# Kernel optimization log

Hardware: AMD Instinct MI355X
Metric: run time of the kernel (lower is better)

The kernel has to match this reference:

```python
import jax, jax.numpy as jnp
import numpy as np

HIDDEN = 2048
NUM_HEADS = 16
HEAD_DIM = HIDDEN // NUM_HEADS


def setup_inputs() -> dict:
    key = jax.random.key(0)
    ks = jax.random.split(key, 5)
    B, S, H = 2, 2048, HIDDEN
    # xavier_uniform bounds
    qkv_bound = float(np.sqrt(6.0 / (H + 3 * H)))
    out_bound = float(np.sqrt(6.0 / (H + H)))
    return {
        "x": jax.random.normal(ks[0], (B, S, H), dtype=jnp.float32),
        "W_qkv": jax.random.uniform(ks[1], (3 * H, H), minval=-qkv_bound, maxval=qkv_bound, dtype=jnp.float32),
        "b_qkv": jnp.zeros((3 * H,), dtype=jnp.float32),
        "W_out": jax.random.uniform(ks[2], (H, H), minval=-out_bound, maxval=out_bound, dtype=jnp.float32),
        "b_out": jnp.zeros((H,), dtype=jnp.float32),
    }


def reference(x, W_qkv, b_qkv, W_out, b_out):
    B, S, H = x.shape
    # fused QKV projection (torch Linear: x @ W.T + b)
    qkv = x @ W_qkv.T + b_qkv                      # (B, S, 3H)
    q, k, v = jnp.split(qkv, 3, axis=-1)
    # (B, S, H) -> (B, N, S, D)
    def to_heads(t):
        return t.reshape(B, S, NUM_HEADS, HEAD_DIM).transpose(0, 2, 1, 3)
    q, k, v = to_heads(q), to_heads(k), to_heads(v)
    scale = HEAD_DIM ** -0.5
    scores = jnp.einsum("bnqd,bnkd->bnqk", q, k) * scale  # (B, N, S, S)
    causal = jnp.triu(jnp.ones((S, S), dtype=bool), k=1)
    scores = jnp.where(causal, -jnp.inf, scores)
    attn = jax.nn.softmax(scores, axis=-1)
    out = jnp.einsum("bnqk,bnkd->bnqd", attn, v)           # (B, N, S, D)
    out = out.transpose(0, 2, 1, 3).reshape(B, S, H)
    return out @ W_out.T + b_out
```

## Files before the change

kernel.cpp:

```cpp
#include <hip/hip_runtime.h>
#include <stdint.h>


using bf16x8 = __attribute__((ext_vector_type(8))) __bf16;
using f32x4  = __attribute__((ext_vector_type(4))) float;

#define S_LEN 2048
#define HID   2048
#define NHEAD 16
#define DHEAD 128
#define QSCALE_L2E (0.08838834764831845f * 1.4426950408889634f)

__device__ __forceinline__ unsigned short f2bf(float f) {
  union { float f; unsigned int u; } c; c.f = f;
  unsigned int u = c.u;
  return (unsigned short)((u + 0x7FFFu + ((u >> 16) & 1u)) >> 16);
}

__device__ __forceinline__ unsigned int pkbf(float a, float b) {
  union { __bf16 h[2]; unsigned int u; } x;
  x.h[0] = (__bf16)a; x.h[1] = (__bf16)b;
  return x.u;
}

__device__ __forceinline__ void gload_lds16(const void* g, void* l) {
  __builtin_amdgcn_global_load_lds(
      (const __attribute__((address_space(1))) unsigned int*)g,
      (__attribute__((address_space(3))) unsigned int*)l, 16, 0, 0);
}

__device__ __forceinline__ f32x4 mfma16(bf16x8 a, bf16x8 b, f32x4 c) {
  return __builtin_amdgcn_mfma_f32_16x16x32_bf16(a, b, c, 0, 0, 0);
}

__device__ __forceinline__ float hmax4(f32x4 v) {
  return fmaxf(fmaxf(v[0], v[1]), fmaxf(v[2], v[3]));
}

__global__ void cvt_bf16(const float* __restrict__ in, unsigned short* __restrict__ out, int n) {
  const int n4 = n >> 2;
  const int stride = gridDim.x * blockDim.x;
  for (int i = blockIdx.x * blockDim.x + threadIdx.x; i < n4; i += stride) {
    float4 v = reinterpret_cast<const float4*>(in)[i];
    ushort4 o;
    o.x = f2bf(v.x); o.y = f2bf(v.y); o.z = f2bf(v.z); o.w = f2bf(v.w);
    reinterpret_cast<ushort4*>(out)[i] = o;
  }
}

template<int EPI>
__global__ __launch_bounds__(256) void gemm_bt(
    const unsigned short* __restrict__ A, const unsigned short* __restrict__ Bw,
    const float* __restrict__ bias, int K, int N,
    unsigned short* __restrict__ q_out, unsigned short* __restrict__ k_out,
    unsigned short* __restrict__ vt_out, float* __restrict__ c_out)
{
  __shared__ char lsA[128 * 128];
  __shared__ char lsB[128 * 128];
  const int tid = threadIdx.x;
  const int l = tid & 63, w = tid >> 6;
  const int wr = w >> 1, wc = w & 1;
  const int bm = blockIdx.x * 128, bn = blockIdx.y * 128;
  const int row16 = l & 15, kg = l >> 4;

  f32x4 acc[4][4] = {};

  for (int k0 = 0; k0 < K; k0 += 64) {
    #pragma unroll
    for (int c = 0; c < 4; ++c) {
      const int o = c * 4096 + tid * 16;
      const int r = o >> 7;
      const int cb = (o & 127) ^ ((r & 7) << 4);
      gload_lds16((const char*)A + ((size_t)(bm + r) * K + k0) * 2 + cb,
                  lsA + c * 4096 + (w << 10));
      gload_lds16((const char*)Bw + ((size_t)(bn + r) * K + k0) * 2 + cb,
                  lsB + c * 4096 + (w << 10));
    }
    __syncthreads();

    #pragma unroll
    for (int h = 0; h < 2; ++h) {
      bf16x8 af[4], bfr[4];
      #pragma unroll
      for (int i = 0; i < 4; ++i) {
        const int ra = wr * 64 + i * 16 + row16;
        af[i]  = *(const bf16x8*)(lsA + ra * 128 + ((h * 64 + kg * 16) ^ ((ra & 7) << 4)));
        const int rb = wc * 64 + i * 16 + row16;
        bfr[i] = *(const bf16x8*)(lsB + rb * 128 + ((h * 64 + kg * 16) ^ ((rb & 7) << 4)));
      }
      #pragma unroll
      for (int i = 0; i < 4; ++i)
        #pragma unroll
        for (int j = 0; j < 4; ++j)
          acc[i][j] = mfma16(af[i], bfr[j], acc[i][j]);
    }
    __syncthreads();
  }

  const int r0 = kg * 4;
  #pragma unroll
  for (int i = 0; i < 4; ++i) {
    const int row = bm + wr * 64 + i * 16 + r0;
    #pragma unroll
    for (int j = 0; j < 4; ++j) {
      const int col = bn + wc * 64 + j * 16 + row16;
      const float bv = bias[col];
      if (EPI == 1) {
        #pragma unroll
        for (int r = 0; r < 4; ++r)
          c_out[(size_t)(row + r) * N + col] = acc[i][j][r] + bv;
      } else {
        const int sec = col >> 11;
        const int within = col & 2047;
        const int head = within >> 7, d = within & 127;
        #pragma unroll
        for (int r = 0; r < 4; ++r) {
          const int rr = row + r;
          const int b = rr >> 11, s = rr & 2047;
          const int bh = b * NHEAD + head;
          const float v = acc[i][j][r] + bv;
          if (sec == 0)
            q_out[((size_t)bh * S_LEN + s) * DHEAD + d] = f2bf(v * QSCALE_L2E);
          else if (sec == 1)
            k_out[((size_t)bh * S_LEN + s) * DHEAD + d] = f2bf(v);
          else
            vt_out[((size_t)bh * DHEAD + d) * S_LEN + s] = f2bf(v);
        }
      }
    }
  }
}

__global__ __launch_bounds__(256, 2) void attn_fwd(
    const unsigned short* __restrict__ Q, const unsigned short* __restrict__ Kk,
    const unsigned short* __restrict__ Vt, unsigned short* __restrict__ O)
{
  __shared__ char lsK[2][64 * 256];
  __shared__ char lsV[2][128 * 128];
  __shared__ char lsP[4][32 * 128];
  const int tid = threadIdx.x, l = tid & 63, w = tid >> 6;
  const int row16 = l & 15, kg = l >> 4;
  const int qb = (blockIdx.y < 16) ? (15 - (int)blockIdx.x) : (int)blockIdx.x;
  const int bh = blockIdx.y;
  const int bidx = bh >> 4, head = bh & 15;

  const char* Qh = (const char*)(Q  + (size_t)bh * S_LEN * DHEAD);
  const char* Kh = (const char*)(Kk + (size_t)bh * S_LEN * DHEAD);
  const char* Vh = (const char*)(Vt + (size_t)bh * DHEAD * S_LEN);

  const int q0w = qb * 128 + w * 32;

  bf16x8 qf[2][4];
  #pragma unroll
  for (int qs = 0; qs < 2; ++qs)
    #pragma unroll
    for (int t = 0; t < 4; ++t)
      qf[qs][t] = *(const bf16x8*)(Qh + ((size_t)(q0w + qs * 16 + row16) * DHEAD + t * 32 + kg * 8) * 2);

  float m[2]  = {-1e30f, -1e30f};
  float ls[2] = {0.f, 0.f};
  f32x4 oacc[2][8] = {};

  const int last = 2 * qb + 1;

#define STAGE(buf, kt_) do {                                                     \
    _Pragma("unroll")                                                            \
    for (int c = 0; c < 4; ++c) {                                                \
      const int o = c * 4096 + tid * 16;                                         \
      const int rk = o >> 8, cbk = (o & 255) ^ ((rk & 7) << 4);                  \
      gload_lds16(Kh + (size_t)((kt_) * 64 + rk) * 256 + cbk,                    \
                  lsK[buf] + c * 4096 + (w << 10));                              \
      const int dv = o >> 7, cbv = (o & 127) ^ ((dv & 7) << 4);                  \
      gload_lds16(Vh + (size_t)dv * 4096 + (size_t)(kt_) * 128 + cbv,            \
                  lsV[buf] + c * 4096 + (w << 10));                              \
    } } while (0)

  STAGE(0, 0);
  __syncthreads();

  int cur = 0;
  for (int kt = 0; ; ++kt) {
    if (kt < last) STAGE(cur ^ 1, kt + 1);

    if (kt * 64 <= q0w + 31) {
      const char* Kc = lsK[cur];
      const char* Vc = lsV[cur];
      char* Pl = lsP[w];

      f32x4 sc[4][2] = {};
      #pragma unroll
      for (int j = 0; j < 4; ++j) {
        const int krow = j * 16 + row16;
        const int sw = (krow & 7) << 4;
        bf16x8 kf[4];
        #pragma unroll
        for (int t = 0; t < 4; ++t)
          kf[t] = *(const bf16x8*)(Kc + krow * 256 + ((t * 64 + kg * 16) ^ sw));
        #pragma unroll
        for (int t = 0; t < 4; ++t) {
          sc[j][0] = mfma16(kf[t], qf[0][t], sc[j][0]);
          sc[j][1] = mfma16(kf[t], qf[1][t], sc[j][1]);
        }
      }

      if (kt >= 2 * qb) {
        #pragma unroll
        for (int j = 0; j < 4; ++j) {
          const int kvb = kt * 64 + j * 16 + kg * 4;
          #pragma unroll
          for (int qs = 0; qs < 2; ++qs) {
            const int qq = q0w + qs * 16 + row16;
            #pragma unroll
            for (int r = 0; r < 4; ++r)
              if (kvb + r > qq) sc[j][qs][r] = -1e30f;
          }
        }
      }

      float pm[2], al[2] = {1.f, 1.f};
      #pragma unroll
      for (int qs = 0; qs < 2; ++qs) {
        float mx = fmaxf(fmaxf(hmax4(sc[0][qs]), hmax4(sc[1][qs])),
                         fmaxf(hmax4(sc[2][qs]), hmax4(sc[3][qs])));
        mx = fmaxf(mx, __shfl_xor(mx, 16, 64));
        mx = fmaxf(mx, __shfl_xor(mx, 32, 64));
        pm[qs] = mx;
      }
      const bool need = (pm[0] > m[0] + 8.f) || (pm[1] > m[1] + 8.f);
      if (__any(need)) {
        const float n0 = fmaxf(m[0], pm[0]), n1 = fmaxf(m[1], pm[1]);
        al[0] = exp2f(m[0] - n0); al[1] = exp2f(m[1] - n1);
        m[0] = n0; m[1] = n1;
        float aq[2][4];
        #pragma unroll
        for (int qs2 = 0; qs2 < 2; ++qs2)
          #pragma unroll
          for (int r = 0; r < 4; ++r)
            aq[qs2][r] = __shfl(al[qs2], kg * 4 + r, 64);
        #pragma unroll
        for (int qs2 = 0; qs2 < 2; ++qs2)
          #pragma unroll
          for (int dt = 0; dt < 8; ++dt)
            #pragma unroll
            for (int r = 0; r < 4; ++r)
              oacc[qs2][dt][r] *= aq[qs2][r];
      }

      #pragma unroll
      for (int qs = 0; qs < 2; ++qs) {
        const int q = qs * 16 + row16;
        const int psw = (q & 7) << 4;
        float ps = 0.f;
        #pragma unroll
        for (int j = 0; j < 4; ++j) {
          const float p0 = exp2f(sc[j][qs][0] - m[qs]);
          const float p1 = exp2f(sc[j][qs][1] - m[qs]);
          const float p2 = exp2f(sc[j][qs][2] - m[qs]);
          const float p3 = exp2f(sc[j][qs][3] - m[qs]);
          ps += (p0 + p1) + (p2 + p3);
          uint2 pw; pw.x = pkbf(p0, p1); pw.y = pkbf(p2, p3);
          *(uint2*)(Pl + q * 128 + ((j * 32 + kg * 8) ^ psw)) = pw;
        }
        ps += __shfl_xor(ps, 16, 64);
        ps += __shfl_xor(ps, 32, 64);
        ls[qs] = ls[qs] * al[qs] + ps;
      }

      bf16x8 pa[2][2];
      #pragma unroll
      for (int qs2 = 0; qs2 < 2; ++qs2) {
        const int q = qs2 * 16 + row16;
        #pragma unroll
        for (int ks = 0; ks < 2; ++ks)
          pa[qs2][ks] = *(const bf16x8*)(Pl + q * 128 + ((ks * 64 + kg * 16) ^ ((q & 7) << 4)));
      }
      #pragma unroll
      for (int dt = 0; dt < 8; ++dt) {
        const int drow = dt * 16 + row16;
        const int vsw = (drow & 7) << 4;
        bf16x8 v0 = *(const bf16x8*)(Vc + drow * 128 + ((kg * 16) ^ vsw));
        bf16x8 v1 = *(const bf16x8*)(Vc + drow * 128 + ((64 + kg * 16) ^ vsw));
        oacc[0][dt] = mfma16(pa[0][0], v0, oacc[0][dt]);
        oacc[0][dt] = mfma16(pa[0][1], v1, oacc[0][dt]);
        oacc[1][dt] = mfma16(pa[1][0], v0, oacc[1][dt]);
        oacc[1][dt] = mfma16(pa[1][1], v1, oacc[1][dt]);
      }
    }

    __syncthreads();
    if (kt == last) break;
    cur ^= 1;
  }
#undef STAGE

  #pragma unroll
  for (int qs2 = 0; qs2 < 2; ++qs2) {
    #pragma unroll
    for (int r = 0; r < 4; ++r) {
      const float lr = __shfl(ls[qs2], kg * 4 + r, 64);
      const float inv = 1.0f / lr;
      const int q = q0w + qs2 * 16 + kg * 4 + r;
      const size_t orow = (size_t)(bidx * S_LEN + q) * HID + (size_t)head * DHEAD;
      #pragma unroll
      for (int dt = 0; dt < 8; ++dt)
        O[orow + dt * 16 + row16] = f2bf(oacc[qs2][dt][r] * inv);
    }
  }
}

extern "C" void kernel_launch(void* const* d_in, const int* in_sizes, int n_in,
                              void* d_out, int out_size, void* d_ws, size_t ws_size,
                              hipStream_t stream) {
  const float* x    = (const float*)d_in[0];
  const float* Wqkv = (const float*)d_in[1];
  const float* bqkv = (const float*)d_in[2];
  const float* Wout = (const float*)d_in[3];
  const float* bout = (const float*)d_in[4];
  float* out = (float*)d_out;

  if (ws_size < 100663296) return;
  char* ws = (char*)d_ws;
  unsigned short* Qb    = (unsigned short*)(ws);
  unsigned short* Kb    = (unsigned short*)(ws + 16777216);
  unsigned short* Vtb   = (unsigned short*)(ws + 2 * 16777216);
  unsigned short* xb    = (unsigned short*)(ws + 3 * 16777216);
  unsigned short* Ob    = xb;
  unsigned short* Wqkvb = (unsigned short*)(ws + 4 * 16777216);
  unsigned short* Woutb = (unsigned short*)(ws + 4 * 16777216 + 25165824);

  cvt_bf16<<<2048, 256, 0, stream>>>(x,    xb,    4096 * 2048);
  cvt_bf16<<<2048, 256, 0, stream>>>(Wqkv, Wqkvb, 6144 * 2048);
  cvt_bf16<<<1024, 256, 0, stream>>>(Wout, Woutb, 2048 * 2048);

  gemm_bt<0><<<dim3(32, 48), 256, 0, stream>>>(xb, Wqkvb, bqkv, 2048, 6144,
                                               Qb, Kb, Vtb, nullptr);
  attn_fwd<<<dim3(16, 32), 256, 0, stream>>>(Qb, Kb, Vtb, Ob);
  gemm_bt<1><<<dim3(32, 16), 256, 0, stream>>>(Ob, Woutb, bout, 2048, 2048,
                                               nullptr, nullptr, nullptr, out);
}
```

Measured before the change: 284.3 us.

## Rewrite projection GEMMs with larger tiles, double-buffered LDS and interleaved MFMA scheduling

Replaces the generic 128x128 single-buffered GEMM with two specialized kernels. The QKV kernel uses 256x256 tiles and the output kernel uses 128x256 tiles, both with 512 threads. Each uses double-buffered LDS staging through global_load_lds, manual waitcnt and barrier scheduling, setprio around MFMA bursts, and a block-index swizzle for L2 locality. The goal is to hide global-memory latency behind compute and cut synchronization stalls in both projection GEMMs. In exchange it needs more LDS and registers per block and hard-codes the K dimension and the fixed problem shapes.

Result: slower. 329.8 us (+16.0%).

```diff
diff --git a/kernel.cpp b/kernel.cpp
--- a/kernel.cpp
+++ b/kernel.cpp
@@ -9,6 +9,7 @@
 #define HID   2048
 #define NHEAD 16
 #define DHEAD 128
+#define KDIM  2048
 #define QSCALE_L2E (0.08838834764831845f * 1.4426950408889634f)
 
 __device__ __forceinline__ unsigned short f2bf(float f) {
@@ -48,85 +49,254 @@
   }
 }
 
-template<int EPI>
-__global__ __launch_bounds__(256) void gemm_bt(
+#define BAR   asm volatile("s_barrier" ::: "memory")
+#define LGKM0 do { asm volatile("s_waitcnt lgkmcnt(0)" ::: "memory"); \
+                   __builtin_amdgcn_sched_barrier(0); } while (0)
+#define VM(n) asm volatile("s_waitcnt vmcnt(" #n ")" ::: "memory")
+#define PRIO1 __builtin_amdgcn_s_setprio(1)
+#define PRIO0 __builtin_amdgcn_s_setprio(0)
+
+__global__ __launch_bounds__(512, 2) void gemm_qkv(
     const unsigned short* __restrict__ A, const unsigned short* __restrict__ Bw,
-    const float* __restrict__ bias, int K, int N,
+    const float* __restrict__ bias,
     unsigned short* __restrict__ q_out, unsigned short* __restrict__ k_out,
-    unsigned short* __restrict__ vt_out, float* __restrict__ c_out)
+    unsigned short* __restrict__ vt_out)
 {
-  __shared__ char lsA[128 * 128];
-  __shared__ char lsB[128 * 128];
-  const int tid = threadIdx.x;
-  const int l = tid & 63, w = tid >> 6;
-  const int wr = w >> 1, wc = w & 1;
-  const int bm = blockIdx.x * 128, bn = blockIdx.y * 128;
+  __shared__ char lsA[2][32768];
+  __shared__ char lsB[2][32768];
+  const int tid = threadIdx.x, l = tid & 63, w = tid >> 6;
+  const int wr = w >> 2, wc = w & 3;
   const int row16 = l & 15, kg = l >> 4;
 
+  const int bid = blockIdx.x;
+  const int swz = (bid & 7) * 48 + (bid >> 3);
+  const int bm = (swz & 15) * 256, bn = (swz >> 4) * 256;
+  const char* Ag = (const char*)A + (size_t)bm * (KDIM * 2);
+  const char* Bg = (const char*)Bw + (size_t)bn * (KDIM * 2);
+
+  f32x4 acc[8][4] = {};
+
+#define STAGE_B(cc) do { _Pragma("unroll")                                     \
+    for (int p = 0; p < 4; ++p) {                                              \
+      const int o = p * 8192 + tid * 16;                                       \
+      const int r = o >> 7;                                                    \
+      const int cb = (o & 127) ^ ((r & 7) << 4);                               \
+      gload_lds16(Bg + (size_t)r * (KDIM * 2) + (cc) * 128 + cb,               \
+                  lsB[(cc) & 1] + o);                                          \
+    } } while (0)
+
+#define STAGE_A(cc, g) do { _Pragma("unroll")                                  \
+    for (int p = 0; p < 2; ++p) {                                              \
+      const int o = p * 8192 + tid * 16;                                       \
+      const int rl = o >> 7;                                                   \
+      const int r = (g) * 128 + rl;                                            \
+      const int cb = (o & 127) ^ ((r & 7) << 4);                               \
+      gload_lds16(Ag + (size_t)r * (KDIM * 2) + (cc) * 128 + cb,               \
+                  lsA[(cc) & 1] + (g) * 16384 + o);                            \
+    } } while (0)
+
+#define RD_A(dst, i0, Ac) do { _Pragma("unroll")                               \
+    for (int i = 0; i < 4; ++i) {                                              \
+      const int m = wr * 128 + ((i0) + i) * 16 + row16;                        \
+      _Pragma("unroll")                                                        \
+      for (int h = 0; h < 2; ++h)                                              \
+        dst[i][h] = *(const bf16x8*)((Ac) + m * 128 +                          \
+                    ((h * 64 + kg * 16) ^ ((m & 7) << 4)));                    \
+    } } while (0)
+
+#define RD_B(dst, j0, Bc) do { _Pragma("unroll")                               \
+    for (int j = 0; j < 2; ++j) {                                              \
+      const int n = wc * 64 + ((j0) + j) * 16 + row16;                         \
+      _Pragma("unroll")                                                        \
+      for (int h = 0; h < 2; ++h)                                              \
+        dst[j][h] = *(const bf16x8*)((Bc) + n * 128 +                          \
+                    ((h * 64 + kg * 16) ^ ((n & 7) << 4)));                    \
+    } } while (0)
+
+#define MM(af, bf, i0, j0) do { _Pragma("unroll")                              \
+    for (int i = 0; i < 4; ++i) { _Pragma("unroll")                            \
+      for (int j = 0; j < 2; ++j) { _Pragma("unroll")                          \
+        for (int h = 0; h < 2; ++h)                                            \
+          acc[(i0) + i][(j0) + j] =                                            \
+            mfma16(af[i][h], bf[j][h], acc[(i0) + i][(j0) + j]);               \
+    } } } while (0)
+
+  STAGE_B(0); STAGE_A(0, 0); STAGE_A(0, 1);
+  STAGE_B(1); STAGE_A(1, 0); STAGE_A(1, 1);
+  VM(4);
+  BAR;
+
+  bf16x8 alo[4][2], ahi[4][2], bA[2][2], bB[2][2];
+  RD_B(bA, 0, lsB[0]);
+  LGKM0;
+
+  #pragma unroll 1
+  for (int t = 0; t < 32; ++t) {
+    const char* Ac = lsA[t & 1];
+    const char* Bc = lsB[t & 1];
+    const char* Bn = lsB[(t + 1) & 1];
+
+    RD_A(alo, 0, Ac);
+    RD_B(bB, 2, Bc);
+    if (t < 30) STAGE_B(t + 2);
+    BAR; LGKM0;
+    PRIO1; MM(alo, bA, 0, 0); PRIO0;
+    BAR;
+
+    RD_A(ahi, 4, Ac);
+    BAR; LGKM0;
+    PRIO1; MM(ahi, bA, 4, 0); PRIO0;
+    BAR;
+
+    if (t < 31) RD_B(bA, 0, Bn);
+    if (t < 30) STAGE_A(t + 2, 0);
+    BAR; LGKM0;
+    PRIO1; MM(alo, bB, 0, 2); PRIO0;
+    BAR;
+
+    if (t < 30) STAGE_A(t + 2, 1);
+    BAR;
+    PRIO1; MM(ahi, bB, 4, 2); PRIO0;
+    if (t < 30)       { VM(4); }
+    else if (t == 30) { VM(0); }
+    BAR;
+  }
+#undef STAGE_B
+#undef STAGE_A
+#undef RD_A
+#undef RD_B
+#undef MM
+
+  #pragma unroll
+  for (int j = 0; j < 4; ++j) {
+    const int col = bn + wc * 64 + j * 16 + row16;
+    const float bvj = bias[col];
+    const int sec = col >> 11;
+    const int within = col & 2047;
+    const int head = within >> 7, d = within & 127;
+    #pragma unroll
+    for (int i = 0; i < 8; ++i) {
+      const int row = bm + wr * 128 + i * 16 + kg * 4;
+      #pragma unroll
+      for (int r = 0; r < 4; ++r) {
+        const int rr = row + r;
+        const int b = rr >> 11, s = rr & 2047;
+        const int bh2 = b * NHEAD + head;
+        const float v = acc[i][j][r] + bvj;
+        if (sec == 0)
+          q_out[((size_t)bh2 * S_LEN + s) * DHEAD + d] = f2bf(v * QSCALE_L2E);
+        else if (sec == 1)
+          k_out[((size_t)bh2 * S_LEN + s) * DHEAD + d] = f2bf(v);
+        else
+          vt_out[((size_t)bh2 * DHEAD + d) * S_LEN + s] = f2bf(v);
+      }
+    }
+  }
+}
+
+__global__ __launch_bounds__(512, 2) void gemm_out(
+    const unsigned short* __restrict__ A, const unsigned short* __restrict__ Bw,
+    const float* __restrict__ bias, float* __restrict__ c_out)
+{
+  __shared__ char lsA[2][16384];
+  __shared__ char lsB[2][32768];
+  const int tid = threadIdx.x, l = tid & 63, w = tid >> 6;
+  const int wr = w >> 2, wc = w & 3;
+  const int row16 = l & 15, kg = l >> 4;
+
+  const int bid = blockIdx.x;
+  const int swz = (bid & 7) * 32 + (bid >> 3);
+  const int bm = (swz & 31) * 128, bn = (swz >> 5) * 256;
+  const char* Ag = (const char*)A + (size_t)bm * (KDIM * 2);
+  const char* Bg = (const char*)Bw + (size_t)bn * (KDIM * 2);
+
   f32x4 acc[4][4] = {};
 
-  for (int k0 = 0; k0 < K; k0 += 64) {
-    #pragma unroll
-    for (int c = 0; c < 4; ++c) {
-      const int o = c * 4096 + tid * 16;
-      const int r = o >> 7;
-      const int cb = (o & 127) ^ ((r & 7) << 4);
-      gload_lds16((const char*)A + ((size_t)(bm + r) * K + k0) * 2 + cb,
-                  lsA + c * 4096 + (w << 10));
-      gload_lds16((const char*)Bw + ((size_t)(bn + r) * K + k0) * 2 + cb,
-                  lsB + c * 4096 + (w << 10));
-    }
-    __syncthreads();
-
-    #pragma unroll
-    for (int h = 0; h < 2; ++h) {
-      bf16x8 af[4], bfr[4];
-      #pragma unroll
-      for (int i = 0; i < 4; ++i) {
-        const int ra = wr * 64 + i * 16 + row16;
-        af[i]  = *(const bf16x8*)(lsA + ra * 128 + ((h * 64 + kg * 16) ^ ((ra & 7) << 4)));
-        const int rb = wc * 64 + i * 16 + row16;
-        bfr[i] = *(const bf16x8*)(lsB + rb * 128 + ((h * 64 + kg * 16) ^ ((rb & 7) << 4)));
-      }
-      #pragma unroll
-      for (int i = 0; i < 4; ++i)
-        #pragma unroll
-        for (int j = 0; j < 4; ++j)
-          acc[i][j] = mfma16(af[i], bfr[j], acc[i][j]);
-    }
-    __syncthreads();
-  }
-
-  const int r0 = kg * 4;
+#define STAGE_B(cc) do { _Pragma("unroll")                                     \
+    for (int p = 0; p < 4; ++p) {                                              \
+      const int o = p * 8192 + tid * 16;                                       \
+      const int r = o >> 7;                                                    \
+      const int cb = (o & 127) ^ ((r & 7) << 4);                               \
+      gload_lds16(Bg + (size_t)r * (KDIM * 2) + (cc) * 128 + cb,               \
+                  lsB[(cc) & 1] + o);                                          \
+    } } while (0)
+
+#define STAGE_A(cc) do { _Pragma("unroll")                                     \
+    for (int p = 0; p < 2; ++p) {                                              \
+      const int o = p * 8192 + tid * 16;                                       \
+      const int r = o >> 7;                                                    \
+      const int cb = (o & 127) ^ ((r & 7) << 4);                               \
+      gload_lds16(Ag + (size_t)r * (KDIM * 2) + (cc) * 128 + cb,               \
+                  lsA[(cc) & 1] + o);                                          \
+    } } while (0)
+
+#define RD_A(dst, Ac) do { _Pragma("unroll")                                   \
+    for (int i = 0; i < 4; ++i) {                                              \
+      const int m = wr * 64 + i * 16 + row16;                                  \
+      _Pragma("unroll")                                                        \
+      for (int h = 0; h < 2; ++h)                                              \
+        dst[i][h] = *(const bf16x8*)((Ac) + m * 128 +                          \
+                    ((h * 64 + kg * 16) ^ ((m & 7) << 4)));                    \
+    } } while (0)
+
+#define RD_B(dst, j0, Bc) do { _Pragma("unroll")                               \
+    for (int j = 0; j < 2; ++j) {                                              \
+      const int n = wc * 64 + ((j0) + j) * 16 + row16;                         \
+      _Pragma("unroll")                                                        \
+      for (int h = 0; h < 2; ++h)                                              \
+        dst[j][h] = *(const bf16x8*)((Bc) + n * 128 +                          \
+                    ((h * 64 + kg * 16) ^ ((n & 7) << 4)));                    \
+    } } while (0)
+
+#define MM(af, bf, j0) do { _Pragma("unroll")                                  \
+    for (int i = 0; i < 4; ++i) { _Pragma("unroll")                            \
+      for (int j = 0; j < 2; ++j) { _Pragma("unroll")                          \
+        for (int h = 0; h < 2; ++h)                                            \
+          acc[i][(j0) + j] = mfma16(af[i][h], bf[j][h], acc[i][(j0) + j]);     \
+    } } } while (0)
+
+  STAGE_B(0); STAGE_A(0); STAGE_A(1);
+  VM(2);
+  BAR;
+
+  bf16x8 af[4][2], b01[2][2], b23[2][2];
+
+  #pragma unroll 1
+  for (int t = 0; t < 32; ++t) {
+    const char* Ac = lsA[t & 1];
+    const char* Bc = lsB[t & 1];
+
+    RD_A(af, Ac);
+    RD_B(b01, 0, Bc);
+    if (t < 31) STAGE_B(t + 1);
+    BAR; LGKM0;
+    PRIO1; MM(af, b01, 0); PRIO0;
+    BAR;
+
+    RD_B(b23, 2, Bc);
+    if (t < 30) STAGE_A(t + 2);
+    BAR; LGKM0;
+    PRIO1; MM(af, b23, 2); PRIO0;
+    if (t < 30)       { VM(2); }
+    else if (t == 30) { VM(0); }
+    BAR;
+  }
+#undef STAGE_B
+#undef STAGE_A
+#undef RD_A
+#undef RD_B
+#undef MM
+
   #pragma unroll
   for (int i = 0; i < 4; ++i) {
-    const int row = bm + wr * 64 + i * 16 + r0;
+    const int row = bm + wr * 64 + i * 16 + kg * 4;
     #pragma unroll
     for (int j = 0; j < 4; ++j) {
       const int col = bn + wc * 64 + j * 16 + row16;
-      const float bv = bias[col];
-      if (EPI == 1) {
-        #pragma unroll
-        for (int r = 0; r < 4; ++r)
-          c_out[(size_t)(row + r) * N + col] = acc[i][j][r] + bv;
-      } else {
-        const int sec = col >> 11;
-        const int within = col & 2047;
-        const int head = within >> 7, d = within & 127;
-        #pragma unroll
-        for (int r = 0; r < 4; ++r) {
-          const int rr = row + r;
-          const int b = rr >> 11, s = rr & 2047;
-          const int bh = b * NHEAD + head;
-          const float v = acc[i][j][r] + bv;
-          if (sec == 0)
-            q_out[((size_t)bh * S_LEN + s) * DHEAD + d] = f2bf(v * QSCALE_L2E);
-          else if (sec == 1)
-            k_out[((size_t)bh * S_LEN + s) * DHEAD + d] = f2bf(v);
-          else
-            vt_out[((size_t)bh * DHEAD + d) * S_LEN + s] = f2bf(v);
-        }
-      }
+      const float bvj = bias[col];
+      #pragma unroll
+      for (int r = 0; r < 4; ++r)
+        c_out[(size_t)(row + r) * HID + col] = acc[i][j][r] + bvj;
     }
   }
 }
@@ -332,9 +502,7 @@
   cvt_bf16<<<2048, 256, 0, stream>>>(Wqkv, Wqkvb, 6144 * 2048);
   cvt_bf16<<<1024, 256, 0, stream>>>(Wout, Woutb, 2048 * 2048);
 
-  gemm_bt<0><<<dim3(32, 48), 256, 0, stream>>>(xb, Wqkvb, bqkv, 2048, 6144,
-                                               Qb, Kb, Vtb, nullptr);
+  gemm_qkv<<<384, 512, 0, stream>>>(xb, Wqkvb, bqkv, Qb, Kb, Vtb);
   attn_fwd<<<dim3(16, 32), 256, 0, stream>>>(Qb, Kb, Vtb, Ob);
-  gemm_bt<1><<<dim3(32, 16), 256, 0, stream>>>(Ob, Woutb, bout, 2048, 2048,
-                                               nullptr, nullptr, nullptr, out);
-}
+  gemm_out<<<256, 512, 0, stream>>>(Ob, Woutb, bout, out);
+}
```
